# Kernel tuning notes

Hardware: AMD Instinct MI355X
Metric: run time of the kernel (lower is better)

Reference implementation:

```python
import jax, jax.numpy as jnp
import numpy as np

# Quantization constants (match init_kwargs)
A_SCALE = 0.05   # activation scale
W_SCALE = 0.01   # weight scale
A_QN, A_QP = -128, 127  # int8 activation clamp range
STRIDE = (2, 2)
PADDING = ((1, 1), (1, 1))
DILATION = (1, 1)


def setup_inputs() -> dict:
    key = jax.random.key(0)
    kx, kw = jax.random.split(key)
    # Input activations [N, C_in, H, W]
    x = jax.random.normal(kx, (32, 256, 56, 56), dtype=jnp.float32)
    # Int4 weights in [-8, 7], stored as int-valued float32 (unpacked form of weight_packed)
    w = jax.random.randint(kw, (256, 256, 3, 3), -8, 8).astype(jnp.float32)
    return {"x": x, "w": w}


def reference(x, w):
    # Activation int8 quantization: round-half-to-even (matches torch.round), clamp to [a_qn, a_qp]
    x_q = jnp.clip(jnp.round(x / A_SCALE), A_QN, A_QP)
    # Int4xInt8 GEMM over unfolded patches == conv on quantized integer values.
    # Values are small ints so fp32 accumulation is exact (|acc| <= 2304*127*8 < 2^24).
    acc = jax.lax.conv_general_dilated(
        x_q, w,
        window_strides=STRIDE,
        padding=PADDING,
        rhs_dilation=DILATION,
        dimension_numbers=("NCHW", "OIHW", "NCHW"),
    )  # [N, C_out, H_out, W_out] = [32, 256, 28, 28]
    # Dequantize: acc_int32 * (a_scale * w_scale); bias=False; out_dtype=float32
    y = acc * (A_SCALE * W_SCALE)
    return y.astype(jnp.float32)
```

## Files before the change

kernel.cpp:

```cpp
#include <hip/hip_runtime.h>
#include <stdint.h>

typedef int v4i __attribute__((ext_vector_type(4)));

#define N_IMG 32
#define C_IN 256
#define H_IN 56
#define W_IN 56
#define C_OUT 256
#define H_OUT 28
#define W_OUT 28
#define H_PAD 58
#define W_PAD 58
#define SP_TOT (N_IMG*H_OUT*W_OUT)

#define XPAD_BYTES ((size_t)N_IMG*H_PAD*W_PAD*C_IN)


__device__ __forceinline__ void glds16(const int8_t* g, int8_t* l) {
    __builtin_amdgcn_global_load_lds(
        (const __attribute__((address_space(1))) void*)g,
        (__attribute__((address_space(3))) void*)l, 16, 0, 0);
}

__global__ __launch_bounds__(256) void quant_kernel(const float* __restrict__ x,
                                                    int8_t* __restrict__ xpad) {
    __shared__ uint32_t ldsu[W_IN * 65];
    const int hp = blockIdx.x, n = blockIdx.y;
    const int t = threadIdx.x;
    int8_t* row = xpad + ((size_t)n * H_PAD + hp) * W_PAD * C_IN;

    if (hp == 0 || hp == H_PAD - 1) {
        #pragma unroll
        for (int i = 0; i < 4; ++i) {
            int idx = i * 256 + t;
            if (idx < 928) *(int4*)(row + idx * 16) = (int4){0, 0, 0, 0};
        }
        return;
    }
    const int h = hp - 1;
    const float* xp = x + (size_t)n * C_IN * H_IN * W_IN + (size_t)h * W_IN;

    const int wv = t >> 6, lane = t & 63;
    const int j = lane >> 4, w4 = lane & 15;
    const int w4c = (w4 < 14) ? w4 : 13;
    const float* base = xp + (size_t)(64 * j) * (H_IN * W_IN) + w4c * 4;

    #pragma unroll
    for (int half = 0; half < 2; ++half) {
        float4 v[8];
        #pragma unroll
        for (int it = 0; it < 8; ++it) {
            const int c4 = (half * 8 + it) * 4 + wv;
            v[it] = *(const float4*)(base + (size_t)c4 * (H_IN * W_IN));
        }
        #pragma unroll
        for (int it = 0; it < 8; ++it) {
            const int c4 = (half * 8 + it) * 4 + wv;
            float f[4] = {v[it].x, v[it].y, v[it].z, v[it].w};
            uint32_t u = 0;
            #pragma unroll
            for (int i = 0; i < 4; ++i) {
                float qv = rintf(f[i] * 20.0f);
                qv = fminf(fmaxf(qv, -128.0f), 127.0f);
                u |= ((uint32_t)((int)qv & 255)) << (8 * i);
            }
            uint32_t p1 = __shfl_xor(u, 16);
            uint32_t tt = (j & 1) ? (((p1 >> 8) & 0x00FF00FFu) | (u & 0xFF00FF00u))
                                  : ((u & 0x00FF00FFu) | ((p1 << 8) & 0xFF00FF00u));
            uint32_t p2 = __shfl_xor(tt, 32);
            uint32_t rr = (j & 2) ? ((p2 >> 16) | (tt & 0xFFFF0000u))
                                  : ((tt & 0x0000FFFFu) | (p2 << 16));
            if (w4 < 14) ldsu[(w4 * 4 + j) * 65 + c4] = rr;
        }
    }
    if (t < 32) {
        int8_t* p = (t < 16) ? (row + t * 16)
                             : (row + (size_t)(W_PAD - 1) * C_IN + (t - 16) * 16);
        *(int4*)p = (int4){0, 0, 0, 0};
    }
    __syncthreads();

    int8_t* op = row + C_IN;
    #pragma unroll
    for (int it = 0; it < 14; ++it) {
        int idx = it * 256 + t;
        int w = idx >> 6, c4 = idx & 63;
        *(uint32_t*)(op + (size_t)w * C_IN + c4 * 4) = ldsu[w * 65 + c4];
    }
}

__global__ __launch_bounds__(256) void wq_kernel(const float* __restrict__ w,
                                                 int8_t* __restrict__ wq) {
    int idx = blockIdx.x * 256 + threadIdx.x;
    int p   = idx & 255;
    int co  = (idx >> 8) & 255;
    int khw = idx >> 16;
    int ci  = 64 * (p & 3) + (p >> 2);
    float v = w[(size_t)(co * C_IN + ci) * 9 + khw];
    wq[idx] = (int8_t)(int)rintf(v);
}

__global__ __launch_bounds__(256) void conv_kernel(const int8_t* __restrict__ xpad,
                                                   const int8_t* __restrict__ wq,
                                                   float* __restrict__ out) {
    __shared__ __align__(16) int8_t lds[32768];
    const int t = threadIdx.x;
    const int wave = t >> 6, lane = t & 63;
    const int q = lane >> 4, s = lane & 15;
    const int co_blk = blockIdx.y * 64;
    const int sp_blk = blockIdx.x * 64;

    const int rl   = t >> 4;
    const int chunk = (t & 15) ^ (rl & 15);
    const int8_t* gw = wq + (size_t)(co_blk + rl) * 256 + chunk * 16;

    const int8_t* ga[4];
    #pragma unroll
    for (int r = 0; r < 4; ++r) {
        int sp = sp_blk + r * 16 + rl;
        int n  = sp / (H_OUT * W_OUT);
        int rm = sp - n * (H_OUT * W_OUT);
        int ho = rm / W_OUT;
        int wo = rm - ho * W_OUT;
        ga[r] = xpad + ((size_t)(n * H_PAD + ho * 2) * W_PAD + wo * 2) * C_IN + chunk * 16;
    }

    const int cw = (wave >> 1) * 32;
    const int sw = (wave & 1) * 32;
    int out_base[2];
    #pragma unroll
    for (int j = 0; j < 2; ++j) {
        int sp = sp_blk + sw + j * 16 + s;
        int n  = sp / (H_OUT * W_OUT);
        int rm = sp - n * (H_OUT * W_OUT);
        int ho = rm / W_OUT;
        int wo = rm - ho * W_OUT;
        out_base[j] = n * (C_OUT * H_OUT * W_OUT) + ho * W_OUT + wo;
    }

    v4i acc[2][2];
    #pragma unroll
    for (int i = 0; i < 2; ++i)
        #pragma unroll
        for (int j = 0; j < 2; ++j)
            acc[i][j] = (v4i){0, 0, 0, 0};

    for (int kh = 0; kh < 3; ++kh) {
        for (int kwv = 0; kwv < 3; ++kwv) {
            __syncthreads();
            const int woff = (kh * 3 + kwv) * (C_OUT * C_IN);
            const int aoff = (kh * W_PAD + kwv) * C_IN;
            #pragma unroll
            for (int r = 0; r < 4; ++r)
                glds16(gw + woff + r * 4096, lds + r * 4096 + t * 16);
            #pragma unroll
            for (int r = 0; r < 4; ++r)
                glds16(ga[r] + aoff, lds + 16384 + r * 4096 + t * 16);
            __syncthreads();

            #pragma unroll
            for (int ks = 0; ks < 4; ++ks) {
                const int st = ((ks * 4 + q) ^ s) * 16;
                v4i a[2], b[2];
                #pragma unroll
                for (int i = 0; i < 2; ++i)
                    a[i] = *(const v4i*)(lds + (cw + i * 16 + s) * 256 + st);
                #pragma unroll
                for (int j = 0; j < 2; ++j)
                    b[j] = *(const v4i*)(lds + 16384 + (sw + j * 16 + s) * 256 + st);
                #pragma unroll
                for (int i = 0; i < 2; ++i)
                    #pragma unroll
                    for (int j = 0; j < 2; ++j)
                        acc[i][j] = __builtin_amdgcn_mfma_i32_16x16x64_i8(
                            a[i], b[j], acc[i][j], 0, 0, 0);
            }
        }
    }

    #pragma unroll
    for (int j = 0; j < 2; ++j) {
        #pragma unroll
        for (int i = 0; i < 2; ++i) {
            const int co0 = co_blk + cw + i * 16 + q * 4;
            #pragma unroll
            for (int r = 0; r < 4; ++r) {
                out[(size_t)out_base[j] + (size_t)(co0 + r) * (H_OUT * W_OUT)] =
                    (float)acc[i][j][r] * 0.0005f;
            }
        }
    }
}

extern "C" void kernel_launch(void* const* d_in, const int* in_sizes, int n_in,
                              void* d_out, int out_size, void* d_ws, size_t ws_size,
                              hipStream_t stream) {
    const float* x = (const float*)d_in[0];
    const float* w = (const float*)d_in[1];
    float* out = (float*)d_out;
    int8_t* xpad = (int8_t*)d_ws;
    int8_t* wqb  = xpad + XPAD_BYTES;

    quant_kernel<<<dim3(H_PAD, N_IMG), 256, 0, stream>>>(x, xpad);
    wq_kernel<<<(9 * C_OUT * C_IN) / 256, 256, 0, stream>>>(w, wqb);
    conv_kernel<<<dim3(SP_TOT / 64, C_OUT / 64), 256, 0, stream>>>(xpad, wqb, out);
}
```

Before: 191.2 us.

## Switch conv to 32x32x32 int8 MFMA with 128-channel output tiles

Replaces the 16x16x64 int8 MFMA tiling with 32x32x32 MFMAs and doubles the output-channel tile per block from 64 to 128, so each wave computes a 64x32 tile with two accumulators. The weight tile per stage grows to 32KB, bringing total LDS to 48KB. The aim is higher arithmetic intensity per LDS read and fewer activation reloads across channel blocks. The trade-off is more LDS and accumulator registers per block and half as many blocks, which may lower occupancy.

```diff
diff --git a/kernel.cpp b/kernel.cpp
--- a/kernel.cpp
+++ b/kernel.cpp
@@ -1,7 +1,8 @@
 #include <hip/hip_runtime.h>
 #include <stdint.h>
 
-typedef int v4i __attribute__((ext_vector_type(4)));
+typedef int v4i  __attribute__((ext_vector_type(4)));
+typedef int v16i __attribute__((ext_vector_type(16)));
 
 #define N_IMG 32
 #define C_IN 256
@@ -104,14 +105,14 @@
 __global__ __launch_bounds__(256) void conv_kernel(const int8_t* __restrict__ xpad,
                                                    const int8_t* __restrict__ wq,
                                                    float* __restrict__ out) {
-    __shared__ __align__(16) int8_t lds[32768];
+    __shared__ __align__(16) int8_t lds[49152];
     const int t = threadIdx.x;
     const int wave = t >> 6, lane = t & 63;
-    const int q = lane >> 4, s = lane & 15;
-    const int co_blk = blockIdx.y * 64;
+    const int l31 = lane & 31, khalf = lane >> 5;
+    const int co_blk = blockIdx.y * 128;
     const int sp_blk = blockIdx.x * 64;
 
-    const int rl   = t >> 4;
+    const int rl    = t >> 4;
     const int chunk = (t & 15) ^ (rl & 15);
     const int8_t* gw = wq + (size_t)(co_blk + rl) * 256 + chunk * 16;
 
@@ -126,25 +127,26 @@
         ga[r] = xpad + ((size_t)(n * H_PAD + ho * 2) * W_PAD + wo * 2) * C_IN + chunk * 16;
     }
 
-    const int cw = (wave >> 1) * 32;
+    const int cw = (wave >> 1) * 64;
     const int sw = (wave & 1) * 32;
-    int out_base[2];
-    #pragma unroll
-    for (int j = 0; j < 2; ++j) {
-        int sp = sp_blk + sw + j * 16 + s;
-        int n  = sp / (H_OUT * W_OUT);
-        int rm = sp - n * (H_OUT * W_OUT);
-        int ho = rm / W_OUT;
-        int wo = rm - ho * W_OUT;
-        out_base[j] = n * (C_OUT * H_OUT * W_OUT) + ho * W_OUT + wo;
+    {
     }
+    const int spo = sp_blk + sw + l31;
+    const int no  = spo / (H_OUT * W_OUT);
+    const int rmo = spo - no * (H_OUT * W_OUT);
+    const int hoo = rmo / W_OUT;
+    const int woo = rmo - hoo * W_OUT;
+    float* outp = out + (size_t)no * (C_OUT * H_OUT * W_OUT) + hoo * W_OUT + woo
+                      + (size_t)(co_blk + cw + 4 * khalf) * (H_OUT * W_OUT);
 
-    v4i acc[2][2];
+    v16i acc[2];
     #pragma unroll
     for (int i = 0; i < 2; ++i)
         #pragma unroll
-        for (int j = 0; j < 2; ++j)
-            acc[i][j] = (v4i){0, 0, 0, 0};
+        for (int r = 0; r < 16; ++r)
+            acc[i][r] = 0;
+
+    const int swz = (l31 & 15);
 
     for (int kh = 0; kh < 3; ++kh) {
         for (int kwv = 0; kwv < 3; ++kwv) {
@@ -152,43 +154,32 @@
             const int woff = (kh * 3 + kwv) * (C_OUT * C_IN);
             const int aoff = (kh * W_PAD + kwv) * C_IN;
             #pragma unroll
-            for (int r = 0; r < 4; ++r)
+            for (int r = 0; r < 8; ++r)
                 glds16(gw + woff + r * 4096, lds + r * 4096 + t * 16);
             #pragma unroll
             for (int r = 0; r < 4; ++r)
-                glds16(ga[r] + aoff, lds + 16384 + r * 4096 + t * 16);
+                glds16(ga[r] + aoff, lds + 32768 + r * 4096 + t * 16);
             __syncthreads();
 
             #pragma unroll
-            for (int ks = 0; ks < 4; ++ks) {
-                const int st = ((ks * 4 + q) ^ s) * 16;
-                v4i a[2], b[2];
+            for (int ks = 0; ks < 8; ++ks) {
+                const int st = ((2 * ks + khalf) ^ swz) * 16;
+                v4i b = *(const v4i*)(lds + 32768 + (sw + l31) * 256 + st);
                 #pragma unroll
-                for (int i = 0; i < 2; ++i)
-                    a[i] = *(const v4i*)(lds + (cw + i * 16 + s) * 256 + st);
-                #pragma unroll
-                for (int j = 0; j < 2; ++j)
-                    b[j] = *(const v4i*)(lds + 16384 + (sw + j * 16 + s) * 256 + st);
-                #pragma unroll
-                for (int i = 0; i < 2; ++i)
-                    #pragma unroll
-                    for (int j = 0; j < 2; ++j)
-                        acc[i][j] = __builtin_amdgcn_mfma_i32_16x16x64_i8(
-                            a[i], b[j], acc[i][j], 0, 0, 0);
+                for (int i = 0; i < 2; ++i) {
+                    v4i a = *(const v4i*)(lds + (cw + 32 * i + l31) * 256 + st);
+                    acc[i] = __builtin_amdgcn_mfma_i32_32x32x32_i8(a, b, acc[i], 0, 0, 0);
+                }
             }
         }
     }
 
     #pragma unroll
-    for (int j = 0; j < 2; ++j) {
+    for (int i = 0; i < 2; ++i) {
         #pragma unroll
-        for (int i = 0; i < 2; ++i) {
-            const int co0 = co_blk + cw + i * 16 + q * 4;
-            #pragma unroll
-            for (int r = 0; r < 4; ++r) {
-                out[(size_t)out_base[j] + (size_t)(co0 + r) * (H_OUT * W_OUT)] =
-                    (float)acc[i][j][r] * 0.0005f;
-            }
+        for (int r = 0; r < 16; ++r) {
+            const int cof = 32 * i + (r & 3) + 8 * (r >> 2);
+            outp[(size_t)cof * (H_OUT * W_OUT)] = (float)acc[i][r] * 0.0005f;
         }
     }
 }
@@ -204,5 +195,5 @@
 
     quant_kernel<<<dim3(H_PAD, N_IMG), 256, 0, stream>>>(x, xpad);
     wq_kernel<<<(9 * C_OUT * C_IN) / 256, 256, 0, stream>>>(w, wqb);
-    conv_kernel<<<dim3(SP_TOT / 64, C_OUT / 64), 256, 0, stream>>>(xpad, wqb, out);
+    conv_kernel<<<dim3(SP_TOT / 64, C_OUT / 128), 256, 0, stream>>>(xpad, wqb, out);
 }
```

New measurement: 194.3 us. No clear change (+1.6%).

## Enlarge conv output tile per wave and split quant kernel over channel halves

Applied to the files above, without the earlier changes.

The conv kernel now uses 2 waves per 128-thread block, each computing a 64x64 tile (128 output channels by 64 spatial positions per block), raising MFMA work per LDS load and halving the number of co-blocks. LDS staging grows to 48 KB, with a new even/odd chunk swizzle for the loads. The quant kernel gains a grid z-dimension that splits channels into two halves, doubling block count and halving LDS per block. The larger accumulator set (64 int regs per lane) increases register pressure and lowers per-block wave count, which may reduce latency hiding.

```diff
diff --git a/kernel.cpp b/kernel.cpp
--- a/kernel.cpp
+++ b/kernel.cpp
@@ -1,7 +1,7 @@
 #include <hip/hip_runtime.h>
 #include <stdint.h>
 
-typedef int v4i __attribute__((ext_vector_type(4)));
+typedef int v4i  __attribute__((ext_vector_type(4)));
 
 #define N_IMG 32
 #define C_IN 256
@@ -25,16 +25,16 @@
 
 __global__ __launch_bounds__(256) void quant_kernel(const float* __restrict__ x,
                                                     int8_t* __restrict__ xpad) {
-    __shared__ uint32_t ldsu[W_IN * 65];
-    const int hp = blockIdx.x, n = blockIdx.y;
+    __shared__ uint32_t ldsu[W_IN * 33];
+    const int hp = blockIdx.x, n = blockIdx.y, z = blockIdx.z;
     const int t = threadIdx.x;
     int8_t* row = xpad + ((size_t)n * H_PAD + hp) * W_PAD * C_IN;
 
     if (hp == 0 || hp == H_PAD - 1) {
         #pragma unroll
-        for (int i = 0; i < 4; ++i) {
+        for (int i = 0; i < 2; ++i) {
             int idx = i * 256 + t;
-            if (idx < 928) *(int4*)(row + idx * 16) = (int4){0, 0, 0, 0};
+            if (idx < 464) *(int4*)(row + z * 7424 + idx * 16) = (int4){0, 0, 0, 0};
         }
         return;
     }
@@ -46,47 +46,44 @@
     const int w4c = (w4 < 14) ? w4 : 13;
     const float* base = xp + (size_t)(64 * j) * (H_IN * W_IN) + w4c * 4;
 
-    #pragma unroll
-    for (int half = 0; half < 2; ++half) {
-        float4 v[8];
-        #pragma unroll
-        for (int it = 0; it < 8; ++it) {
-            const int c4 = (half * 8 + it) * 4 + wv;
-            v[it] = *(const float4*)(base + (size_t)c4 * (H_IN * W_IN));
-        }
-        #pragma unroll
-        for (int it = 0; it < 8; ++it) {
-            const int c4 = (half * 8 + it) * 4 + wv;
-            float f[4] = {v[it].x, v[it].y, v[it].z, v[it].w};
-            uint32_t u = 0;
-            #pragma unroll
-            for (int i = 0; i < 4; ++i) {
-                float qv = rintf(f[i] * 20.0f);
-                qv = fminf(fmaxf(qv, -128.0f), 127.0f);
-                u |= ((uint32_t)((int)qv & 255)) << (8 * i);
-            }
-            uint32_t p1 = __shfl_xor(u, 16);
-            uint32_t tt = (j & 1) ? (((p1 >> 8) & 0x00FF00FFu) | (u & 0xFF00FF00u))
-                                  : ((u & 0x00FF00FFu) | ((p1 << 8) & 0xFF00FF00u));
-            uint32_t p2 = __shfl_xor(tt, 32);
-            uint32_t rr = (j & 2) ? ((p2 >> 16) | (tt & 0xFFFF0000u))
-                                  : ((tt & 0x0000FFFFu) | (p2 << 16));
-            if (w4 < 14) ldsu[(w4 * 4 + j) * 65 + c4] = rr;
-        }
-    }
-    if (t < 32) {
-        int8_t* p = (t < 16) ? (row + t * 16)
-                             : (row + (size_t)(W_PAD - 1) * C_IN + (t - 16) * 16);
+    float4 v[8];
+    #pragma unroll
+    for (int it = 0; it < 8; ++it) {
+        const int c4 = 32 * z + it * 4 + wv;
+        v[it] = *(const float4*)(base + (size_t)c4 * (H_IN * W_IN));
+    }
+    #pragma unroll
+    for (int it = 0; it < 8; ++it) {
+        const int c4l = it * 4 + wv;
+        float f[4] = {v[it].x, v[it].y, v[it].z, v[it].w};
+        uint32_t u = 0;
+        #pragma unroll
+        for (int i = 0; i < 4; ++i) {
+            float qv = rintf(f[i] * 20.0f);
+            qv = fminf(fmaxf(qv, -128.0f), 127.0f);
+            u |= ((uint32_t)((int)qv & 255)) << (8 * i);
+        }
+        uint32_t p1 = __shfl_xor(u, 16);
+        uint32_t tt = (j & 1) ? (((p1 >> 8) & 0x00FF00FFu) | (u & 0xFF00FF00u))
+                              : ((u & 0x00FF00FFu) | ((p1 << 8) & 0xFF00FF00u));
+        uint32_t p2 = __shfl_xor(tt, 32);
+        uint32_t rr = (j & 2) ? ((p2 >> 16) | (tt & 0xFFFF0000u))
+                              : ((tt & 0x0000FFFFu) | (p2 << 16));
+        if (w4 < 14) ldsu[(w4 * 4 + j) * 33 + c4l] = rr;
+    }
+    if (t < 16) {
+        int pix = t >> 3;
+        int8_t* p = row + (size_t)pix * (W_PAD - 1) * C_IN + z * 128 + (t & 7) * 16;
         *(int4*)p = (int4){0, 0, 0, 0};
     }
     __syncthreads();
 
-    int8_t* op = row + C_IN;
-    #pragma unroll
-    for (int it = 0; it < 14; ++it) {
+    int8_t* op = row + C_IN + z * 128;
+    #pragma unroll
+    for (int it = 0; it < 7; ++it) {
         int idx = it * 256 + t;
-        int w = idx >> 6, c4 = idx & 63;
-        *(uint32_t*)(op + (size_t)w * C_IN + c4 * 4) = ldsu[w * 65 + c4];
+        int w = idx >> 5, c4l = idx & 31;
+        *(uint32_t*)(op + (size_t)w * C_IN + c4l * 4) = ldsu[w * 33 + c4l];
     }
 }
 
@@ -101,50 +98,51 @@
     wq[idx] = (int8_t)(int)rintf(v);
 }
 
-__global__ __launch_bounds__(256) void conv_kernel(const int8_t* __restrict__ xpad,
+__global__ __launch_bounds__(128) void conv_kernel(const int8_t* __restrict__ xpad,
                                                    const int8_t* __restrict__ wq,
                                                    float* __restrict__ out) {
-    __shared__ __align__(16) int8_t lds[32768];
+    __shared__ __align__(16) int8_t lds[49152];
     const int t = threadIdx.x;
     const int wave = t >> 6, lane = t & 63;
     const int q = lane >> 4, s = lane & 15;
-    const int co_blk = blockIdx.y * 64;
+    const int co_blk = blockIdx.y * 128;
     const int sp_blk = blockIdx.x * 64;
 
-    const int rl   = t >> 4;
-    const int chunk = (t & 15) ^ (rl & 15);
-    const int8_t* gw = wq + (size_t)(co_blk + rl) * 256 + chunk * 16;
-
-    const int8_t* ga[4];
-    #pragma unroll
-    for (int r = 0; r < 4; ++r) {
-        int sp = sp_blk + r * 16 + rl;
+    const int rl  = t >> 4;
+    const int ch0 = (t & 15) ^ rl;
+    const int8_t* gwE = wq + (size_t)(co_blk + rl) * 256 + ch0 * 16;
+    const int8_t* gwO = wq + (size_t)(co_blk + rl) * 256 + (ch0 ^ 8) * 16;
+
+    int aofs[8];
+    #pragma unroll
+    for (int p = 0; p < 8; ++p) {
+        int sp = sp_blk + p * 8 + rl;
         int n  = sp / (H_OUT * W_OUT);
         int rm = sp - n * (H_OUT * W_OUT);
         int ho = rm / W_OUT;
         int wo = rm - ho * W_OUT;
-        ga[r] = xpad + ((size_t)(n * H_PAD + ho * 2) * W_PAD + wo * 2) * C_IN + chunk * 16;
-    }
-
-    const int cw = (wave >> 1) * 32;
-    const int sw = (wave & 1) * 32;
-    int out_base[2];
-    #pragma unroll
-    for (int j = 0; j < 2; ++j) {
-        int sp = sp_blk + sw + j * 16 + s;
+        aofs[p] = ((n * H_PAD + ho * 2) * W_PAD + wo * 2) * C_IN
+                + (ch0 ^ (8 * (p & 1))) * 16;
+    }
+
+    int out_base[4];
+    #pragma unroll
+    for (int jj = 0; jj < 4; ++jj) {
+        int sp = sp_blk + jj * 16 + s;
         int n  = sp / (H_OUT * W_OUT);
         int rm = sp - n * (H_OUT * W_OUT);
         int ho = rm / W_OUT;
         int wo = rm - ho * W_OUT;
-        out_base[j] = n * (C_OUT * H_OUT * W_OUT) + ho * W_OUT + wo;
-    }
-
-    v4i acc[2][2];
-    #pragma unroll
-    for (int i = 0; i < 2; ++i)
-        #pragma unroll
-        for (int j = 0; j < 2; ++j)
-            acc[i][j] = (v4i){0, 0, 0, 0};
+        out_base[jj] = n * (C_OUT * H_OUT * W_OUT) + ho * W_OUT + wo;
+    }
+    const int cw = wave * 64;
+
+    v4i acc[4][4];
+    #pragma unroll
+    for (int i = 0; i < 4; ++i)
+        #pragma unroll
+        for (int jj = 0; jj < 4; ++jj)
+            acc[i][jj] = (v4i){0, 0, 0, 0};
 
     for (int kh = 0; kh < 3; ++kh) {
         for (int kwv = 0; kwv < 3; ++kwv) {
@@ -152,42 +150,44 @@
             const int woff = (kh * 3 + kwv) * (C_OUT * C_IN);
             const int aoff = (kh * W_PAD + kwv) * C_IN;
             #pragma unroll
-            for (int r = 0; r < 4; ++r)
-                glds16(gw + woff + r * 4096, lds + r * 4096 + t * 16);
-            #pragma unroll
-            for (int r = 0; r < 4; ++r)
-                glds16(ga[r] + aoff, lds + 16384 + r * 4096 + t * 16);
+            for (int p = 0; p < 16; ++p)
+                glds16(((p & 1) ? gwO : gwE) + woff + p * 2048,
+                       lds + p * 2048 + t * 16);
+            #pragma unroll
+            for (int p = 0; p < 8; ++p)
+                glds16(xpad + aofs[p] + aoff,
+                       lds + 32768 + p * 2048 + t * 16);
             __syncthreads();
 
             #pragma unroll
             for (int ks = 0; ks < 4; ++ks) {
                 const int st = ((ks * 4 + q) ^ s) * 16;
-                v4i a[2], b[2];
+                v4i a[4], b[4];
                 #pragma unroll
-                for (int i = 0; i < 2; ++i)
+                for (int i = 0; i < 4; ++i)
                     a[i] = *(const v4i*)(lds + (cw + i * 16 + s) * 256 + st);
                 #pragma unroll
-                for (int j = 0; j < 2; ++j)
-                    b[j] = *(const v4i*)(lds + 16384 + (sw + j * 16 + s) * 256 + st);
+                for (int jj = 0; jj < 4; ++jj)
+                    b[jj] = *(const v4i*)(lds + 32768 + (jj * 16 + s) * 256 + st);
                 #pragma unroll
-                for (int i = 0; i < 2; ++i)
+                for (int i = 0; i < 4; ++i)
                     #pragma unroll
-                    for (int j = 0; j < 2; ++j)
-                        acc[i][j] = __builtin_amdgcn_mfma_i32_16x16x64_i8(
-                            a[i], b[j], acc[i][j], 0, 0, 0);
+                    for (int jj = 0; jj < 4; ++jj)
+                        acc[i][jj] = __builtin_amdgcn_mfma_i32_16x16x64_i8(
+                            a[i], b[jj], acc[i][jj], 0, 0, 0);
             }
         }
     }
 
     #pragma unroll
-    for (int j = 0; j < 2; ++j) {
-        #pragma unroll
-        for (int i = 0; i < 2; ++i) {
+    for (int jj = 0; jj < 4; ++jj) {
+        #pragma unroll
+        for (int i = 0; i < 4; ++i) {
             const int co0 = co_blk + cw + i * 16 + q * 4;
             #pragma unroll
             for (int r = 0; r < 4; ++r) {
-                out[(size_t)out_base[j] + (size_t)(co0 + r) * (H_OUT * W_OUT)] =
-                    (float)acc[i][j][r] * 0.0005f;
+                out[(size_t)out_base[jj] + (size_t)(co0 + r) * (H_OUT * W_OUT)] =
+                    (float)acc[i][jj][r] * 0.0005f;
             }
         }
     }
@@ -202,7 +202,7 @@
     int8_t* xpad = (int8_t*)d_ws;
     int8_t* wqb  = xpad + XPAD_BYTES;
 
-    quant_kernel<<<dim3(H_PAD, N_IMG), 256, 0, stream>>>(x, xpad);
+    quant_kernel<<<dim3(H_PAD, N_IMG, 2), 256, 0, stream>>>(x, xpad);
     wq_kernel<<<(9 * C_OUT * C_IN) / 256, 256, 0, stream>>>(w, wqb);
-    conv_kernel<<<dim3(SP_TOT / 64, C_OUT / 64), 256, 0, stream>>>(xpad, wqb, out);
-}
+    conv_kernel<<<dim3(SP_TOT / 64, C_OUT / 128), 128, 0, stream>>>(xpad, wqb, out);
+}
```

Measured after the change: 195.6 us. 1.02x slower.
